# Kernel optimization log

Hardware: AMD Instinct MI355X
Metric: run time of the kernel (lower is better)

The kernel has to match this reference:

```python
import jax, jax.numpy as jnp
import numpy as np

B, T, C, H, RANK = 4, 2048, 1024, 16, 8


def _lora_linear(x, W, b, A, Bm):
    # loralib-style: y = x W^T + b + (x A^T) B^T  (scaling alpha/r = 1)
    return x @ W.T + b + (x @ A.T) @ Bm.T


def setup_inputs() -> dict:
    key = jax.random.key(0)
    ks = jax.random.split(key, 6)
    s_in = 1.0 / np.sqrt(C)
    return {
        "x": jax.random.normal(ks[0], (B, T, C), jnp.float32),
        "c_attn_w": jax.random.normal(ks[1], (3 * C, C), jnp.float32) * s_in,
        "c_attn_b": jnp.zeros((3 * C,), jnp.float32),
        "c_attn_A": jax.random.normal(ks[2], (RANK, C), jnp.float32) * s_in,
        "c_attn_B": jnp.zeros((3 * C, RANK), jnp.float32),
        "c_proj_w": jax.random.normal(ks[3], (C, C), jnp.float32) * s_in,
        "c_proj_b": jnp.zeros((C,), jnp.float32),
        "c_proj_A": jax.random.normal(ks[4], (RANK, C), jnp.float32) * s_in,
        "c_proj_B": jnp.zeros((C, RANK), jnp.float32),
        "n_head": H,
    }


def reference(x, c_attn_w, c_attn_b, c_attn_A, c_attn_B,
              c_proj_w, c_proj_b, c_proj_A, c_proj_B, n_head):
    Bsz, Tlen, Cd = x.shape
    d = Cd // n_head
    qkv = _lora_linear(x, c_attn_w, c_attn_b, c_attn_A, c_attn_B)  # [B,T,3C]
    q, k, v = jnp.split(qkv, 3, axis=2)
    query, key_out = q, k  # returned pre-reshape, as in torch
    # [B, H, T, d]
    qh = q.reshape(Bsz, Tlen, n_head, d).transpose(0, 2, 1, 3)
    kh = k.reshape(Bsz, Tlen, n_head, d).transpose(0, 2, 1, 3)
    vh = v.reshape(Bsz, Tlen, n_head, d).transpose(0, 2, 1, 3)
    att = jnp.einsum('bhqd,bhkd->bhqk', qh, kh) * (1.0 / np.sqrt(d))
    causal = jnp.tril(jnp.ones((Tlen, Tlen), bool))
    att = jnp.where(causal[None, None], att, -jnp.inf)
    att = jax.nn.softmax(att, axis=-1)
    y = jnp.einsum('bhqk,bhkd->bhqd', att, vh)
    y = y.transpose(0, 2, 1, 3).reshape(Bsz, Tlen, Cd)
    out = _lora_linear(y, c_proj_w, c_proj_b, c_proj_A, c_proj_B)
    return out, query, key_out
```

## Files before the change

kernel.cpp:

```cpp
#include <hip/hip_runtime.h>
#include <stdint.h>

#define T_LEN 2048
#define C_DIM 1024
#define NHEAD 16
#define DHEAD 64
#define QOFF  8388608L
#define KOFF  16777216L
#define SCALE_LOG2 0.18033688011112042f

typedef float f32x4 __attribute__((ext_vector_type(4)));
typedef short bf16x8 __attribute__((ext_vector_type(8)));
typedef short s16x4 __attribute__((ext_vector_type(4)));
typedef unsigned short u16;

__device__ __forceinline__ float b2f(u16 h) {
  union { uint32_t u; float f; } v; v.u = ((uint32_t)h) << 16; return v.f;
}
__device__ __forceinline__ u16 f2b(float f) {
  union { float f; uint32_t u; } v; v.f = f;
  uint32_t r = v.u + 0x7fffu + ((v.u >> 16) & 1u);
  return (u16)(r >> 16);
}
__device__ __forceinline__ u16 f2b_tr(float f) {
  union { float f; uint32_t u; } v; v.f = f;
  return (u16)(v.u >> 16);
}
__device__ __forceinline__ void async16(const u16* g, u16* l) {
  __builtin_amdgcn_global_load_lds((const __attribute__((address_space(1))) void*)g,
                                   (__attribute__((address_space(3))) void*)l, 16, 0, 0);
}

__global__ __launch_bounds__(256) void convert_x(const float* __restrict__ xin,
                                                 u16* __restrict__ xc) {
  long i = ((long)blockIdx.x * 256 + threadIdx.x) * 4;
  f32x4 v = *(const f32x4*)(xin + i);
  s16x4 r;
  r[0] = (short)f2b(v[0]); r[1] = (short)f2b(v[1]);
  r[2] = (short)f2b(v[2]); r[3] = (short)f2b(v[3]);
  *(s16x4*)(xc + i) = r;
}

__global__ __launch_bounds__(256) void prep_weff(const float* __restrict__ W,
                                                 const float* __restrict__ Bm,
                                                 const float* __restrict__ Aw,
                                                 u16* __restrict__ out, int total) {
  int i = blockIdx.x * 256 + threadIdx.x;
  if (i >= total) return;
  int n = i >> 10, k = i & 1023;
  float acc = W[i];
#pragma unroll
  for (int r = 0; r < 8; r++) acc += Bm[n * 8 + r] * Aw[r * 1024 + k];
  out[i] = f2b(acc);
}

template <int MODE>
__global__ __launch_bounds__(256) void gemm_bt(const u16* __restrict__ A,
                                               const u16* __restrict__ Bt,
                                               const float* __restrict__ bias,
                                               float* __restrict__ outf,
                                               u16* __restrict__ kc,
                                               u16* __restrict__ vblk, int K) {
  __shared__ __align__(16) u16 ldsA[128 * 32];
  __shared__ __align__(16) u16 ldsB[128 * 32];
  const int t = threadIdx.x;
  const int lane = t & 63, l15 = lane & 15, quad = lane >> 4, w = t >> 6;
  const int wr = (w >> 1) * 64, wc = (w & 1) * 64;
  const long rowA = (long)blockIdx.y * 128;
  const long rowB = (long)blockIdx.x * 128;
  const int srow = t >> 2, scol = (t & 3) * 8;

  f32x4 acc[4][4];
#pragma unroll
  for (int i = 0; i < 4; i++)
#pragma unroll
    for (int j = 0; j < 4; j++) { f32x4 z = {0.f, 0.f, 0.f, 0.f}; acc[i][j] = z; }

  const u16* Ab = A + rowA * K;
  const u16* Bb = Bt + rowB * K;
  for (int k0 = 0; k0 < K; k0 += 32) {
    __syncthreads();
    async16(Ab + (long)srow * K + k0 + scol, &ldsA[t * 8]);
    async16(Ab + (long)(srow + 64) * K + k0 + scol, &ldsA[2048 + t * 8]);
    async16(Bb + (long)srow * K + k0 + scol, &ldsB[t * 8]);
    async16(Bb + (long)(srow + 64) * K + k0 + scol, &ldsB[2048 + t * 8]);
    __syncthreads();
    bf16x8 af[4], bfr[4];
#pragma unroll
    for (int g = 0; g < 4; g++) {
      af[g]  = *(const bf16x8*)&ldsA[(wr + g * 16 + l15) * 32 + quad * 8];
      bfr[g] = *(const bf16x8*)&ldsB[(wc + g * 16 + l15) * 32 + quad * 8];
    }
#pragma unroll
    for (int i = 0; i < 4; i++)
#pragma unroll
      for (int j = 0; j < 4; j++)
        acc[i][j] = __builtin_amdgcn_mfma_f32_16x16x32_bf16(af[i], bfr[j], acc[i][j], 0, 0, 0);
  }

#pragma unroll
  for (int i = 0; i < 4; i++) {
#pragma unroll
    for (int j = 0; j < 4; j++) {
      int n = (int)rowB + wc + j * 16 + l15;
      float bv = bias[n];
#pragma unroll
      for (int r = 0; r < 4; r++) {
        int m = (int)rowA + wr + i * 16 + quad * 4 + r;
        float val = acc[i][j][r] + bv;
        if constexpr (MODE == 1) {
          outf[(long)m * C_DIM + n] = val;
        } else {
          int sec = n >> 10;
          int nc = n & 1023;
          int h = nc >> 6, dd = nc & 63;
          int bb = m >> 11, tt = m & 2047;
          int bh = bb * NHEAD + h;
          if (sec == 0) {
            outf[QOFF + (long)m * C_DIM + nc] = val;
          } else if (sec == 1) {
            outf[KOFF + (long)m * C_DIM + nc] = val;
            kc[(long)bh * (T_LEN * 64) + (long)tt * 64 + dd] = f2b(val);
          } else {
            vblk[(long)bh * (T_LEN * 64) + (long)(tt >> 6) * 4096 + dd * 64 + (tt & 63)] = f2b(val);
          }
        }
      }
    }
  }
}

__global__ __launch_bounds__(256) void flash_attn(const float* __restrict__ qsec,
                                                  const u16* __restrict__ kc,
                                                  const u16* __restrict__ vblk,
                                                  u16* __restrict__ yb) {
  __shared__ __align__(16) u16 ldsK[64 * 64];
  __shared__ __align__(16) u16 ldsV[64 * 64];
  __shared__ __align__(16) u16 plds[4][32 * 72];
  const int t = threadIdx.x;
  const int lane = t & 63, l15 = lane & 15, quad = lane >> 4, w = t >> 6;
  const int qt = 15 - (blockIdx.x >> 6);
  const int bh = blockIdx.x & 63;
  const int q0 = qt * 128;
  const int bb = bh >> 4, h = bh & 15;

  const float* Qb = qsec + ((long)bb * T_LEN + q0 + w * 32) * C_DIM + h * DHEAD;
  bf16x8 qf[2][2];
#pragma unroll
  for (int rg = 0; rg < 2; rg++)
#pragma unroll
    for (int kk = 0; kk < 2; kk++) {
      const float* p = Qb + (long)(rg * 16 + l15) * C_DIM + kk * 32 + quad * 8;
      f32x4 a = *(const f32x4*)p, b = *(const f32x4*)(p + 4);
      bf16x8 r;
      r[0] = (short)f2b(a[0] * SCALE_LOG2); r[1] = (short)f2b(a[1] * SCALE_LOG2);
      r[2] = (short)f2b(a[2] * SCALE_LOG2); r[3] = (short)f2b(a[3] * SCALE_LOG2);
      r[4] = (short)f2b(b[0] * SCALE_LOG2); r[5] = (short)f2b(b[1] * SCALE_LOG2);
      r[6] = (short)f2b(b[2] * SCALE_LOG2); r[7] = (short)f2b(b[3] * SCALE_LOG2);
      qf[rg][kk] = r;
    }

  bf16x8 ones;
#pragma unroll
  for (int j = 0; j < 8; j++) ones[j] = (short)0x3F80;

  f32x4 o[2][4];
  f32x4 ls[2];
#pragma unroll
  for (int rg = 0; rg < 2; rg++) {
#pragma unroll
    for (int cg = 0; cg < 4; cg++) { f32x4 z = {0.f, 0.f, 0.f, 0.f}; o[rg][cg] = z; }
    f32x4 z = {0.f, 0.f, 0.f, 0.f}; ls[rg] = z;
  }

  const u16* kcb = kc + (long)bh * (T_LEN * 64);
  const u16* vbb = vblk + (long)bh * (T_LEN * 64);
  const int l0 = t, l1 = 256 + t;
  const int s0c = ((l0 >> 3) * 8 + ((l0 & 7) ^ ((l0 >> 3) & 7))) * 8;
  const int s1c = ((l1 >> 3) * 8 + ((l1 & 7) ^ ((l1 >> 3) & 7))) * 8;

  const int qminw = q0 + w * 32;
  const int nkt = (q0 + 128) >> 6;
  for (int kt = 0; kt < nkt; kt++) {
    const int kb0 = kt * 64;
    __syncthreads();
    {
      const u16* ks = kcb + (long)kb0 * 64;
      const u16* vs = vbb + (long)kt * 4096;
      async16(ks + s0c, &ldsK[l0 * 8]);
      async16(ks + s1c, &ldsK[l1 * 8]);
      async16(vs + s0c, &ldsV[l0 * 8]);
      async16(vs + s1c, &ldsV[l1 * 8]);
    }
    __syncthreads();
    if (kb0 > qminw + 31) continue;

    f32x4 s[2][4];
#pragma unroll
    for (int rg = 0; rg < 2; rg++)
#pragma unroll
      for (int kg = 0; kg < 4; kg++) { f32x4 z = {0.f, 0.f, 0.f, 0.f}; s[rg][kg] = z; }
#pragma unroll
    for (int kg = 0; kg < 4; kg++) {
      int row = kg * 16 + l15, sw = row & 7;
      bf16x8 kf0 = *(const bf16x8*)&ldsK[row * 64 + ((quad ^ sw) * 8)];
      bf16x8 kf1 = *(const bf16x8*)&ldsK[row * 64 + (((4 + quad) ^ sw) * 8)];
#pragma unroll
      for (int rg = 0; rg < 2; rg++) {
        s[rg][kg] = __builtin_amdgcn_mfma_f32_16x16x32_bf16(qf[rg][0], kf0, s[rg][kg], 0, 0, 0);
        s[rg][kg] = __builtin_amdgcn_mfma_f32_16x16x32_bf16(qf[rg][1], kf1, s[rg][kg], 0, 0, 0);
      }
    }
    const bool needMask = (kb0 + 63) > qminw;
#pragma unroll
    for (int rg = 0; rg < 2; rg++) {
#pragma unroll
      for (int r = 0; r < 4; r++) {
        float v0 = s[rg][0][r], v1 = s[rg][1][r], v2 = s[rg][2][r], v3 = s[rg][3][r];
        if (needMask) {
          int qrow = qminw + rg * 16 + quad * 4 + r;
          if (kb0 + l15 > qrow)      v0 = -3.0e38f;
          if (kb0 + 16 + l15 > qrow) v1 = -3.0e38f;
          if (kb0 + 32 + l15 > qrow) v2 = -3.0e38f;
          if (kb0 + 48 + l15 > qrow) v3 = -3.0e38f;
        }
        int prow = rg * 16 + quad * 4 + r;
        plds[w][prow * 72 + l15]      = f2b_tr(exp2f(v0));
        plds[w][prow * 72 + 16 + l15] = f2b_tr(exp2f(v1));
        plds[w][prow * 72 + 32 + l15] = f2b_tr(exp2f(v2));
        plds[w][prow * 72 + 48 + l15] = f2b_tr(exp2f(v3));
      }
    }
    asm volatile("s_waitcnt lgkmcnt(0)" ::: "memory");
    bf16x8 pf[2][2];
#pragma unroll
    for (int rg = 0; rg < 2; rg++)
#pragma unroll
      for (int kk = 0; kk < 2; kk++)
        pf[rg][kk] = *(const bf16x8*)&plds[w][(rg * 16 + l15) * 72 + kk * 32 + quad * 8];
#pragma unroll
    for (int rg = 0; rg < 2; rg++) {
      ls[rg] = __builtin_amdgcn_mfma_f32_16x16x32_bf16(pf[rg][0], ones, ls[rg], 0, 0, 0);
      ls[rg] = __builtin_amdgcn_mfma_f32_16x16x32_bf16(pf[rg][1], ones, ls[rg], 0, 0, 0);
    }
#pragma unroll
    for (int cg = 0; cg < 4; cg++) {
      int row = cg * 16 + l15, sw = row & 7;
      bf16x8 vf0 = *(const bf16x8*)&ldsV[row * 64 + ((quad ^ sw) * 8)];
      bf16x8 vf1 = *(const bf16x8*)&ldsV[row * 64 + (((4 + quad) ^ sw) * 8)];
#pragma unroll
      for (int rg = 0; rg < 2; rg++) {
        o[rg][cg] = __builtin_amdgcn_mfma_f32_16x16x32_bf16(pf[rg][0], vf0, o[rg][cg], 0, 0, 0);
        o[rg][cg] = __builtin_amdgcn_mfma_f32_16x16x32_bf16(pf[rg][1], vf1, o[rg][cg], 0, 0, 0);
      }
    }
  }
#pragma unroll
  for (int rg = 0; rg < 2; rg++) {
#pragma unroll
    for (int r = 0; r < 4; r++) {
      float inv = 1.0f / ls[rg][r];
      int tt = q0 + w * 32 + rg * 16 + quad * 4 + r;
      long base = ((long)bb * T_LEN + tt) * C_DIM + h * DHEAD;
#pragma unroll
      for (int cg = 0; cg < 4; cg++)
        yb[base + cg * 16 + l15] = f2b(o[rg][cg][r] * inv);
    }
  }
}

extern "C" void kernel_launch(void* const* d_in, const int* in_sizes, int n_in,
                              void* d_out, int out_size, void* d_ws, size_t ws_size,
                              hipStream_t stream) {
  const float* x  = (const float*)d_in[0];
  const float* w1 = (const float*)d_in[1];
  const float* b1 = (const float*)d_in[2];
  const float* A1 = (const float*)d_in[3];
  const float* B1 = (const float*)d_in[4];
  const float* w2 = (const float*)d_in[5];
  const float* b2 = (const float*)d_in[6];
  const float* A2 = (const float*)d_in[7];
  const float* B2 = (const float*)d_in[8];
  float* outf = (float*)d_out;
  u16* outb16 = (u16*)d_out;

  u16* ws  = (u16*)d_ws;
  u16* w2e = ws;
  u16* w1e = ws + 1048576;
  u16* xc  = ws + 4194304;
  u16* yb  = ws + 1048576;
  u16* vblk = outb16;
  u16* kcp  = outb16 + 8388608;

  convert_x<<<8192, 256, 0, stream>>>(x, xc);
  prep_weff<<<12288, 256, 0, stream>>>(w1, B1, A1, w1e, 3072 * 1024);
  prep_weff<<<4096, 256, 0, stream>>>(w2, B2, A2, w2e, 1024 * 1024);
  gemm_bt<0><<<dim3(24, 64), 256, 0, stream>>>(xc, w1e, b1, outf, kcp, vblk, 1024);
  flash_attn<<<1024, 256, 0, stream>>>(outf + QOFF, kcp, vblk, yb);
  gemm_bt<1><<<dim3(8, 64), 256, 0, stream>>>(yb, w2e, b2, outf, nullptr, nullptr, 1024);
}
```

Baseline: 352.5 us.

## Replace QKV GEMM with 256x256 double-buffered, swizzled, pipelined MFMA kernel

```diff
diff --git a/kernel.cpp b/kernel.cpp
--- a/kernel.cpp
+++ b/kernel.cpp
@@ -30,6 +30,8 @@
   __builtin_amdgcn_global_load_lds((const __attribute__((address_space(1))) void*)g,
                                    (__attribute__((address_space(3))) void*)l, 16, 0, 0);
 }
+
+#define MFMA16 __builtin_amdgcn_mfma_f32_16x16x32_bf16
 
 __global__ __launch_bounds__(256) void convert_x(const float* __restrict__ xin,
                                                  u16* __restrict__ xc) {
@@ -52,6 +54,160 @@
 #pragma unroll
   for (int r = 0; r < 8; r++) acc += Bm[n * 8 + r] * Aw[r * 1024 + k];
   out[i] = f2b(acc);
+}
+
+__global__ __launch_bounds__(512, 2) void gemm256_qkv(const u16* __restrict__ A,
+                                                      const u16* __restrict__ Bt,
+                                                      const float* __restrict__ bias,
+                                                      float* __restrict__ outf,
+                                                      u16* __restrict__ kc,
+                                                      u16* __restrict__ vblk) {
+  __shared__ __align__(16) u16 ldsA[2][256 * 64];
+  __shared__ __align__(16) u16 ldsB[2][256 * 64];
+  const int t = threadIdx.x;
+  const int lane = t & 63, l15 = lane & 15, quad = lane >> 4;
+  const int w = t >> 6, wm = w >> 2, wn = w & 3;
+  const int flat = blockIdx.x;
+  const int swz = (flat & 7) * 48 + (flat >> 3);
+  const int bx = swz % 12, by = swz / 12;
+  const long rowA = (long)by * 256, rowB = (long)bx * 256;
+  const u16* Ab = A + rowA * C_DIM;
+  const u16* Bb = Bt + rowB * C_DIM;
+
+  const int sr = t >> 3;
+  const int sk = ((t & 7) ^ (sr & 7)) * 8;
+  const int sdst = t * 8;
+
+#define STAGE_A(tt, gi) async16(Ab + (long)((gi) * 64 + sr) * C_DIM + (tt) * 64 + sk, \
+                                &ldsA[(tt) & 1][(gi) * 4096 + sdst])
+#define STAGE_B(tt, gi) async16(Bb + (long)((gi) * 64 + sr) * C_DIM + (tt) * 64 + sk, \
+                                &ldsB[(tt) & 1][(gi) * 4096 + sdst])
+
+  f32x4 acc[8][4];
+#pragma unroll
+  for (int i = 0; i < 8; i++)
+#pragma unroll
+    for (int j = 0; j < 4; j++) { f32x4 z = {0.f, 0.f, 0.f, 0.f}; acc[i][j] = z; }
+
+#pragma unroll
+  for (int gi = 0; gi < 4; gi++) { STAGE_A(0, gi); STAGE_B(0, gi); }
+#pragma unroll
+  for (int gi = 0; gi < 4; gi++) { STAGE_A(1, gi); STAGE_B(1, gi); }
+  asm volatile("s_waitcnt vmcnt(8)" ::: "memory");
+  __builtin_amdgcn_s_barrier();
+
+  const int arow = wm * 128 + l15;
+  const int brow = wn * 64 + l15;
+  const int xsw = l15 & 7;
+
+  bf16x8 af[4][2], bf[4][2];
+
+  for (int kt = 0; kt < 16; kt++) {
+    const u16* lA = ldsA[kt & 1];
+    const u16* lB = ldsB[kt & 1];
+    const bool st = (kt < 14);
+
+#pragma unroll
+    for (int rg = 0; rg < 4; rg++)
+#pragma unroll
+      for (int k = 0; k < 2; k++)
+        af[rg][k] = *(const bf16x8*)&lA[(arow + rg * 16) * 64 + (((k * 4 + quad) ^ xsw) * 8)];
+#pragma unroll
+    for (int cg = 0; cg < 2; cg++)
+#pragma unroll
+      for (int k = 0; k < 2; k++)
+        bf[cg][k] = *(const bf16x8*)&lB[(brow + cg * 16) * 64 + (((k * 4 + quad) ^ xsw) * 8)];
+    __builtin_amdgcn_s_barrier();
+    __builtin_amdgcn_s_setprio(1);
+#pragma unroll
+    for (int rg = 0; rg < 4; rg++)
+#pragma unroll
+      for (int cg = 0; cg < 2; cg++) {
+        acc[rg][cg] = MFMA16(af[rg][0], bf[cg][0], acc[rg][cg], 0, 0, 0);
+        acc[rg][cg] = MFMA16(af[rg][1], bf[cg][1], acc[rg][cg], 0, 0, 0);
+      }
+    __builtin_amdgcn_s_setprio(0);
+    __builtin_amdgcn_s_barrier();
+
+#pragma unroll
+    for (int cg = 2; cg < 4; cg++)
+#pragma unroll
+      for (int k = 0; k < 2; k++)
+        bf[cg][k] = *(const bf16x8*)&lB[(brow + cg * 16) * 64 + (((k * 4 + quad) ^ xsw) * 8)];
+    if (st) { STAGE_A(kt + 2, 0); STAGE_A(kt + 2, 2); }
+    __builtin_amdgcn_s_barrier();
+    __builtin_amdgcn_s_setprio(1);
+#pragma unroll
+    for (int rg = 0; rg < 4; rg++)
+#pragma unroll
+      for (int cg = 2; cg < 4; cg++) {
+        acc[rg][cg] = MFMA16(af[rg][0], bf[cg][0], acc[rg][cg], 0, 0, 0);
+        acc[rg][cg] = MFMA16(af[rg][1], bf[cg][1], acc[rg][cg], 0, 0, 0);
+      }
+    __builtin_amdgcn_s_setprio(0);
+    __builtin_amdgcn_s_barrier();
+
+#pragma unroll
+    for (int rg = 0; rg < 4; rg++)
+#pragma unroll
+      for (int k = 0; k < 2; k++)
+        af[rg][k] = *(const bf16x8*)&lA[(arow + 64 + rg * 16) * 64 + (((k * 4 + quad) ^ xsw) * 8)];
+    if (st) { STAGE_B(kt + 2, 0); STAGE_B(kt + 2, 1); STAGE_B(kt + 2, 2); STAGE_B(kt + 2, 3); }
+    __builtin_amdgcn_s_barrier();
+    __builtin_amdgcn_s_setprio(1);
+#pragma unroll
+    for (int rg = 0; rg < 4; rg++)
+#pragma unroll
+      for (int cg = 0; cg < 2; cg++) {
+        acc[4 + rg][cg] = MFMA16(af[rg][0], bf[cg][0], acc[4 + rg][cg], 0, 0, 0);
+        acc[4 + rg][cg] = MFMA16(af[rg][1], bf[cg][1], acc[4 + rg][cg], 0, 0, 0);
+      }
+    __builtin_amdgcn_s_setprio(0);
+    __builtin_amdgcn_s_barrier();
+
+    if (st) {
+      STAGE_A(kt + 2, 1); STAGE_A(kt + 2, 3);
+      asm volatile("s_waitcnt vmcnt(8)" ::: "memory");
+    } else {
+      asm volatile("s_waitcnt vmcnt(0)" ::: "memory");
+    }
+    __builtin_amdgcn_s_barrier();
+    __builtin_amdgcn_s_setprio(1);
+#pragma unroll
+    for (int rg = 0; rg < 4; rg++)
+#pragma unroll
+      for (int cg = 2; cg < 4; cg++) {
+        acc[4 + rg][cg] = MFMA16(af[rg][0], bf[cg][0], acc[4 + rg][cg], 0, 0, 0);
+        acc[4 + rg][cg] = MFMA16(af[rg][1], bf[cg][1], acc[4 + rg][cg], 0, 0, 0);
+      }
+    __builtin_amdgcn_s_setprio(0);
+    __builtin_amdgcn_s_barrier();
+  }
+
+  const int sec = bx >> 2;
+#pragma unroll
+  for (int rg = 0; rg < 8; rg++) {
+#pragma unroll
+    for (int cg = 0; cg < 4; cg++) {
+      int n = (int)rowB + wn * 64 + cg * 16 + l15;
+      float bv = bias[n];
+      int nc = n & 1023, h = nc >> 6, dd = nc & 63;
+#pragma unroll
+      for (int r = 0; r < 4; r++) {
+        int m = (int)rowA + wm * 128 + rg * 16 + quad * 4 + r;
+        float val = acc[rg][cg][r] + bv;
+        int bb = m >> 11, tt2 = m & 2047, bh = bb * NHEAD + h;
+        if (sec == 0) {
+          outf[QOFF + (long)m * C_DIM + nc] = val;
+        } else if (sec == 1) {
+          outf[KOFF + (long)m * C_DIM + nc] = val;
+          kc[(long)bh * (T_LEN * 64) + (long)tt2 * 64 + dd] = f2b(val);
+        } else {
+          vblk[(long)bh * (T_LEN * 64) + (long)(tt2 >> 6) * 4096 + dd * 64 + (tt2 & 63)] = f2b(val);
+        }
+      }
+    }
+  }
 }
 
 template <int MODE>
@@ -95,7 +251,7 @@
     for (int i = 0; i < 4; i++)
 #pragma unroll
       for (int j = 0; j < 4; j++)
-        acc[i][j] = __builtin_amdgcn_mfma_f32_16x16x32_bf16(af[i], bfr[j], acc[i][j], 0, 0, 0);
+        acc[i][j] = MFMA16(af[i], bfr[j], acc[i][j], 0, 0, 0);
   }
 
 #pragma unroll
@@ -207,8 +363,8 @@
       bf16x8 kf1 = *(const bf16x8*)&ldsK[row * 64 + (((4 + quad) ^ sw) * 8)];
 #pragma unroll
       for (int rg = 0; rg < 2; rg++) {
-        s[rg][kg] = __builtin_amdgcn_mfma_f32_16x16x32_bf16(qf[rg][0], kf0, s[rg][kg], 0, 0, 0);
-        s[rg][kg] = __builtin_amdgcn_mfma_f32_16x16x32_bf16(qf[rg][1], kf1, s[rg][kg], 0, 0, 0);
+        s[rg][kg] = MFMA16(qf[rg][0], kf0, s[rg][kg], 0, 0, 0);
+        s[rg][kg] = MFMA16(qf[rg][1], kf1, s[rg][kg], 0, 0, 0);
       }
     }
     const bool needMask = (kb0 + 63) > qminw;
@@ -240,8 +396,8 @@
         pf[rg][kk] = *(const bf16x8*)&plds[w][(rg * 16 + l15) * 72 + kk * 32 + quad * 8];
 #pragma unroll
     for (int rg = 0; rg < 2; rg++) {
-      ls[rg] = __builtin_amdgcn_mfma_f32_16x16x32_bf16(pf[rg][0], ones, ls[rg], 0, 0, 0);
-      ls[rg] = __builtin_amdgcn_mfma_f32_16x16x32_bf16(pf[rg][1], ones, ls[rg], 0, 0, 0);
+      ls[rg] = MFMA16(pf[rg][0], ones, ls[rg], 0, 0, 0);
+      ls[rg] = MFMA16(pf[rg][1], ones, ls[rg], 0, 0, 0);
     }
 #pragma unroll
     for (int cg = 0; cg < 4; cg++) {
@@ -250,8 +406,8 @@
       bf16x8 vf1 = *(const bf16x8*)&ldsV[row * 64 + (((4 + quad) ^ sw) * 8)];
 #pragma unroll
       for (int rg = 0; rg < 2; rg++) {
-        o[rg][cg] = __builtin_amdgcn_mfma_f32_16x16x32_bf16(pf[rg][0], vf0, o[rg][cg], 0, 0, 0);
-        o[rg][cg] = __builtin_amdgcn_mfma_f32_16x16x32_bf16(pf[rg][1], vf1, o[rg][cg], 0, 0, 0);
+        o[rg][cg] = MFMA16(pf[rg][0], vf0, o[rg][cg], 0, 0, 0);
+        o[rg][cg] = MFMA16(pf[rg][1], vf1, o[rg][cg], 0, 0, 0);
       }
     }
   }
@@ -295,7 +451,7 @@
   convert_x<<<8192, 256, 0, stream>>>(x, xc);
   prep_weff<<<12288, 256, 0, stream>>>(w1, B1, A1, w1e, 3072 * 1024);
   prep_weff<<<4096, 256, 0, stream>>>(w2, B2, A2, w2e, 1024 * 1024);
-  gemm_bt<0><<<dim3(24, 64), 256, 0, stream>>>(xc, w1e, b1, outf, kcp, vblk, 1024);
+  gemm256_qkv<<<384, 512, 0, stream>>>(xc, w1e, b1, outf, kcp, vblk);
   flash_attn<<<1024, 256, 0, stream>>>(outf + QOFF, kcp, vblk, yb);
   gemm_bt<1><<<dim3(8, 64), 256, 0, stream>>>(yb, w2e, b2, outf, nullptr, nullptr, 1024);
 }
```

After: 351.5 us. No clear change (-0.3%).

## Double-buffer K/V tiles in flash attention to overlap loads with compute

Applied to the files above, without the earlier changes.

```diff
diff --git a/kernel.cpp b/kernel.cpp
--- a/kernel.cpp
+++ b/kernel.cpp
@@ -30,6 +30,8 @@
   __builtin_amdgcn_global_load_lds((const __attribute__((address_space(1))) void*)g,
                                    (__attribute__((address_space(3))) void*)l, 16, 0, 0);
 }
+
+#define MFMA16 __builtin_amdgcn_mfma_f32_16x16x32_bf16
 
 __global__ __launch_bounds__(256) void convert_x(const float* __restrict__ xin,
                                                  u16* __restrict__ xc) {
@@ -95,7 +97,7 @@
     for (int i = 0; i < 4; i++)
 #pragma unroll
       for (int j = 0; j < 4; j++)
-        acc[i][j] = __builtin_amdgcn_mfma_f32_16x16x32_bf16(af[i], bfr[j], acc[i][j], 0, 0, 0);
+        acc[i][j] = MFMA16(af[i], bfr[j], acc[i][j], 0, 0, 0);
   }
 
 #pragma unroll
@@ -134,8 +136,8 @@
                                                   const u16* __restrict__ kc,
                                                   const u16* __restrict__ vblk,
                                                   u16* __restrict__ yb) {
-  __shared__ __align__(16) u16 ldsK[64 * 64];
-  __shared__ __align__(16) u16 ldsV[64 * 64];
+  __shared__ __align__(16) u16 ldsK[2][64 * 64];
+  __shared__ __align__(16) u16 ldsV[2][64 * 64];
   __shared__ __align__(16) u16 plds[4][32 * 72];
   const int t = threadIdx.x;
   const int lane = t & 63, l15 = lane & 15, quad = lane >> 4, w = t >> 6;
@@ -181,80 +183,91 @@
 
   const int qminw = q0 + w * 32;
   const int nkt = (q0 + 128) >> 6;
+
+#define KV_STAGE(kt_, b_) do {                                        \
+    const u16* ks_ = kcb + (long)(kt_) * 4096;                        \
+    const u16* vs_ = vbb + (long)(kt_) * 4096;                        \
+    async16(ks_ + s0c, &ldsK[b_][l0 * 8]);                            \
+    async16(ks_ + s1c, &ldsK[b_][l1 * 8]);                            \
+    async16(vs_ + s0c, &ldsV[b_][l0 * 8]);                            \
+    async16(vs_ + s1c, &ldsV[b_][l1 * 8]);                            \
+  } while (0)
+
+  KV_STAGE(0, 0);
+  asm volatile("s_waitcnt vmcnt(0)" ::: "memory");
+  __builtin_amdgcn_s_barrier();
+
   for (int kt = 0; kt < nkt; kt++) {
     const int kb0 = kt * 64;
-    __syncthreads();
-    {
-      const u16* ks = kcb + (long)kb0 * 64;
-      const u16* vs = vbb + (long)kt * 4096;
-      async16(ks + s0c, &ldsK[l0 * 8]);
-      async16(ks + s1c, &ldsK[l1 * 8]);
-      async16(vs + s0c, &ldsV[l0 * 8]);
-      async16(vs + s1c, &ldsV[l1 * 8]);
-    }
-    __syncthreads();
-    if (kb0 > qminw + 31) continue;
-
-    f32x4 s[2][4];
-#pragma unroll
-    for (int rg = 0; rg < 2; rg++)
-#pragma unroll
-      for (int kg = 0; kg < 4; kg++) { f32x4 z = {0.f, 0.f, 0.f, 0.f}; s[rg][kg] = z; }
-#pragma unroll
-    for (int kg = 0; kg < 4; kg++) {
-      int row = kg * 16 + l15, sw = row & 7;
-      bf16x8 kf0 = *(const bf16x8*)&ldsK[row * 64 + ((quad ^ sw) * 8)];
-      bf16x8 kf1 = *(const bf16x8*)&ldsK[row * 64 + (((4 + quad) ^ sw) * 8)];
+    const int cur = kt & 1;
+    if (kt + 1 < nkt) KV_STAGE(kt + 1, cur ^ 1);
+
+    if (kb0 <= qminw + 31) {
+      f32x4 s[2][4];
+#pragma unroll
+      for (int rg = 0; rg < 2; rg++)
+#pragma unroll
+        for (int kg = 0; kg < 4; kg++) { f32x4 z = {0.f, 0.f, 0.f, 0.f}; s[rg][kg] = z; }
+#pragma unroll
+      for (int kg = 0; kg < 4; kg++) {
+        int row = kg * 16 + l15, sw = row & 7;
+        bf16x8 kf0 = *(const bf16x8*)&ldsK[cur][row * 64 + ((quad ^ sw) * 8)];
+        bf16x8 kf1 = *(const bf16x8*)&ldsK[cur][row * 64 + (((4 + quad) ^ sw) * 8)];
+#pragma unroll
+        for (int rg = 0; rg < 2; rg++) {
+          s[rg][kg] = MFMA16(qf[rg][0], kf0, s[rg][kg], 0, 0, 0);
+          s[rg][kg] = MFMA16(qf[rg][1], kf1, s[rg][kg], 0, 0, 0);
+        }
+      }
+      const bool needMask = (kb0 + 63) > qminw;
 #pragma unroll
       for (int rg = 0; rg < 2; rg++) {
-        s[rg][kg] = __builtin_amdgcn_mfma_f32_16x16x32_bf16(qf[rg][0], kf0, s[rg][kg], 0, 0, 0);
-        s[rg][kg] = __builtin_amdgcn_mfma_f32_16x16x32_bf16(qf[rg][1], kf1, s[rg][kg], 0, 0, 0);
-      }
-    }
-    const bool needMask = (kb0 + 63) > qminw;
-#pragma unroll
-    for (int rg = 0; rg < 2; rg++) {
-#pragma unroll
-      for (int r = 0; r < 4; r++) {
-        float v0 = s[rg][0][r], v1 = s[rg][1][r], v2 = s[rg][2][r], v3 = s[rg][3][r];
-        if (needMask) {
-          int qrow = qminw + rg * 16 + quad * 4 + r;
-          if (kb0 + l15 > qrow)      v0 = -3.0e38f;
-          if (kb0 + 16 + l15 > qrow) v1 = -3.0e38f;
-          if (kb0 + 32 + l15 > qrow) v2 = -3.0e38f;
-          if (kb0 + 48 + l15 > qrow) v3 = -3.0e38f;
+#pragma unroll
+        for (int r = 0; r < 4; r++) {
+          float v0 = s[rg][0][r], v1 = s[rg][1][r], v2 = s[rg][2][r], v3 = s[rg][3][r];
+          if (needMask) {
+            int qrow = qminw + rg * 16 + quad * 4 + r;
+            if (kb0 + l15 > qrow)      v0 = -3.0e38f;
+            if (kb0 + 16 + l15 > qrow) v1 = -3.0e38f;
+            if (kb0 + 32 + l15 > qrow) v2 = -3.0e38f;
+            if (kb0 + 48 + l15 > qrow) v3 = -3.0e38f;
+          }
+          int prow = rg * 16 + quad * 4 + r;
+          plds[w][prow * 72 + l15]      = f2b_tr(exp2f(v0));
+          plds[w][prow * 72 + 16 + l15] = f2b_tr(exp2f(v1));
+          plds[w][prow * 72 + 32 + l15] = f2b_tr(exp2f(v2));
+          plds[w][prow * 72 + 48 + l15] = f2b_tr(exp2f(v3));
         }
-        int prow = rg * 16 + quad * 4 + r;
-        plds[w][prow * 72 + l15]      = f2b_tr(exp2f(v0));
-        plds[w][prow * 72 + 16 + l15] = f2b_tr(exp2f(v1));
-        plds[w][prow * 72 + 32 + l15] = f2b_tr(exp2f(v2));
-        plds[w][prow * 72 + 48 + l15] = f2b_tr(exp2f(v3));
-      }
-    }
-    asm volatile("s_waitcnt lgkmcnt(0)" ::: "memory");
-    bf16x8 pf[2][2];
-#pragma unroll
-    for (int rg = 0; rg < 2; rg++)
-#pragma unroll
-      for (int kk = 0; kk < 2; kk++)
-        pf[rg][kk] = *(const bf16x8*)&plds[w][(rg * 16 + l15) * 72 + kk * 32 + quad * 8];
-#pragma unroll
-    for (int rg = 0; rg < 2; rg++) {
-      ls[rg] = __builtin_amdgcn_mfma_f32_16x16x32_bf16(pf[rg][0], ones, ls[rg], 0, 0, 0);
-      ls[rg] = __builtin_amdgcn_mfma_f32_16x16x32_bf16(pf[rg][1], ones, ls[rg], 0, 0, 0);
-    }
-#pragma unroll
-    for (int cg = 0; cg < 4; cg++) {
-      int row = cg * 16 + l15, sw = row & 7;
-      bf16x8 vf0 = *(const bf16x8*)&ldsV[row * 64 + ((quad ^ sw) * 8)];
-      bf16x8 vf1 = *(const bf16x8*)&ldsV[row * 64 + (((4 + quad) ^ sw) * 8)];
+      }
+      asm volatile("s_waitcnt lgkmcnt(0)" ::: "memory");
+      bf16x8 pf[2][2];
+#pragma unroll
+      for (int rg = 0; rg < 2; rg++)
+#pragma unroll
+        for (int kk = 0; kk < 2; kk++)
+          pf[rg][kk] = *(const bf16x8*)&plds[w][(rg * 16 + l15) * 72 + kk * 32 + quad * 8];
 #pragma unroll
       for (int rg = 0; rg < 2; rg++) {
-        o[rg][cg] = __builtin_amdgcn_mfma_f32_16x16x32_bf16(pf[rg][0], vf0, o[rg][cg], 0, 0, 0);
-        o[rg][cg] = __builtin_amdgcn_mfma_f32_16x16x32_bf16(pf[rg][1], vf1, o[rg][cg], 0, 0, 0);
-      }
-    }
-  }
+        ls[rg] = MFMA16(pf[rg][0], ones, ls[rg], 0, 0, 0);
+        ls[rg] = MFMA16(pf[rg][1], ones, ls[rg], 0, 0, 0);
+      }
+#pragma unroll
+      for (int cg = 0; cg < 4; cg++) {
+        int row = cg * 16 + l15, sw = row & 7;
+        bf16x8 vf0 = *(const bf16x8*)&ldsV[cur][row * 64 + ((quad ^ sw) * 8)];
+        bf16x8 vf1 = *(const bf16x8*)&ldsV[cur][row * 64 + (((4 + quad) ^ sw) * 8)];
+#pragma unroll
+        for (int rg = 0; rg < 2; rg++) {
+          o[rg][cg] = MFMA16(pf[rg][0], vf0, o[rg][cg], 0, 0, 0);
+          o[rg][cg] = MFMA16(pf[rg][1], vf1, o[rg][cg], 0, 0, 0);
+        }
+      }
+    }
+
+    asm volatile("s_waitcnt vmcnt(0)" ::: "memory");
+    __builtin_amdgcn_s_barrier();
+  }
+
 #pragma unroll
   for (int rg = 0; rg < 2; rg++) {
 #pragma unroll
```

Result: no change. 350.6 us (-0.5%).
